# Kernel tuning notes

Hardware: AMD Instinct MI355X
Metric: run time of the kernel (lower is better)

The kernel has to match this reference:

```python
import jax, jax.numpy as jnp
import numpy as np

V = 49152      # HEALPix nside=64 pixel count
B = 2
FIN = 32
FOUT = 64
K = 8          # Chebyshev kernel_size
DEG = 8        # neighbors per pixel (plus self-loop -> 9 nnz/row)
G = 8          # GroupNorm num_groups
EPS = 1e-5
SLOPE = 0.1    # LeakyReLU negative slope


def setup_inputs() -> dict:
    key = jax.random.key(0)
    ks = jax.random.split(key, 4)
    rng = np.random.default_rng(0)
    # sparse Laplacian in COO: 8 random neighbors + self-loop per node
    row = np.repeat(np.arange(V, dtype=np.int32), DEG + 1)
    nbrs = rng.integers(0, V, size=(V, DEG))
    col = np.concatenate([nbrs, np.arange(V)[:, None]], axis=1).astype(np.int32).reshape(-1)
    vals = (rng.standard_normal(V * (DEG + 1)).astype(np.float32)) * 0.1
    x = jax.random.normal(ks[0], (B, V, FIN), dtype=jnp.float32)
    W1 = jax.random.normal(ks[1], (K, FIN, FOUT), dtype=jnp.float32) * 0.05
    W2 = jax.random.normal(ks[2], (K, FOUT, FOUT), dtype=jnp.float32) * 0.05
    Wr = jax.random.normal(ks[3], (K, FIN, FOUT), dtype=jnp.float32) * 0.05
    zeros = jnp.zeros((FOUT,), dtype=jnp.float32)
    ones = jnp.ones((FOUT,), dtype=jnp.float32)
    return {
        "x": x,
        "lap_vals": jnp.asarray(vals),
        "lap_row": jnp.asarray(row),
        "lap_col": jnp.asarray(col),
        "W1": W1, "b1": zeros, "g1": ones, "be1": zeros,
        "W2": W2, "b2": zeros, "g2": ones, "be2": zeros,
        "Wr": Wr, "br": zeros,
    }


def _spmm(vals, row, col, z):
    # L @ z for COO Laplacian; z: [V, D]
    return jax.ops.segment_sum(vals[:, None] * z[col], row, num_segments=V)


def _cheb_conv(x, vals, row, col, W, b):
    # x: [B, V, Fin], W: [K, Fin, Fout] -> [B, V, Fout]
    Bb, Vv, F = x.shape
    x0 = jnp.transpose(x, (1, 0, 2)).reshape(Vv, Bb * F)  # [V, B*F]
    xs = [x0, _spmm(vals, row, col, x0)]
    for _ in range(K - 2):
        xs.append(2.0 * _spmm(vals, row, col, xs[-1]) - xs[-2])
    Xk = jnp.stack(xs, 0).reshape(K, Vv, Bb, F)
    Xk = jnp.transpose(Xk, (2, 1, 0, 3))  # [B, V, K, F]
    return jnp.einsum('bvkf,kfo->bvo', Xk, W) + b


def _group_norm(x, gamma, beta):
    # equivalent to nn.GroupNorm applied on x.permute(0,2,1): normalize over (C/G, V)
    Bb, Vv, C = x.shape
    xg = x.reshape(Bb, Vv, G, C // G)
    mu = xg.mean(axis=(1, 3), keepdims=True)
    var = xg.var(axis=(1, 3), keepdims=True)
    xn = ((xg - mu) * jax.lax.rsqrt(var + EPS)).reshape(Bb, Vv, C)
    return xn * gamma + beta


def _block(x, vals, row, col, W, b, gamma, beta):
    h = _cheb_conv(x, vals, row, col, W, b)
    h = _group_norm(h, gamma, beta)
    return jax.nn.leaky_relu(h, SLOPE)  # out_channels > 1 -> LeakyReLU(0.1)


def reference(x, lap_vals, lap_row, lap_col, W1, b1, g1, be1, W2, b2, g2, be2, Wr, br):
    h = _block(x, lap_vals, lap_row, lap_col, W1, b1, g1, be1)
    h = _block(h, lap_vals, lap_row, lap_col, W2, b2, g2, be2)
    res = _cheb_conv(x, lap_vals, lap_row, lap_col, Wr, br)  # in != out -> res_conv
    return h + res
```

## Files before the change

### kernel.cpp

```cpp
#include <hip/hip_runtime.h>
#include <hip/hip_bf16.h>

#define V 49152
#define NNZ 9
#define EPSV 1e-5f
#define SLOPE 0.1f
#define RST 68

typedef __attribute__((ext_vector_type(8))) short bf16x8;
typedef __attribute__((ext_vector_type(4))) float f32x4;

__device__ __forceinline__ float lo2f(unsigned u) { return __uint_as_float(u << 16); }
__device__ __forceinline__ float hi2f(unsigned u) { return __uint_as_float(u & 0xffff0000u); }
__device__ __forceinline__ unsigned short f2us(float f) {
    __hip_bfloat16 h = __float2bfloat16(f);
    return *(unsigned short*)&h;
}
__device__ __forceinline__ unsigned pk2(float a, float b) {
    return ((unsigned)f2us(a)) | (((unsigned)f2us(b)) << 16);
}
__device__ __forceinline__ void fma8(float* t, float a, uint4 u) {
    t[0] += a * lo2f(u.x); t[1] += a * hi2f(u.x);
    t[2] += a * lo2f(u.y); t[3] += a * hi2f(u.y);
    t[4] += a * lo2f(u.z); t[5] += a * hi2f(u.z);
    t[6] += a * lo2f(u.w); t[7] += a * hi2f(u.w);
}
__device__ __forceinline__ void fold8(float* t, uint4 p) {
    t[0] = 2.f*t[0] - lo2f(p.x); t[1] = 2.f*t[1] - hi2f(p.x);
    t[2] = 2.f*t[2] - lo2f(p.y); t[3] = 2.f*t[3] - hi2f(p.y);
    t[4] = 2.f*t[4] - lo2f(p.z); t[5] = 2.f*t[5] - hi2f(p.z);
    t[6] = 2.f*t[6] - lo2f(p.w); t[7] = 2.f*t[7] - hi2f(p.w);
}
__device__ __forceinline__ uint4 pack8(const float* t) {
    uint4 r;
    r.x = pk2(t[0], t[1]); r.y = pk2(t[2], t[3]);
    r.z = pk2(t[4], t[5]); r.w = pk2(t[6], t[7]);
    return r;
}
__device__ __forceinline__ void gnleaky8(uint4 u, const float* scl, const float* sft, float* y) {
    float e[8] = { lo2f(u.x), hi2f(u.x), lo2f(u.y), hi2f(u.y),
                   lo2f(u.z), hi2f(u.z), lo2f(u.w), hi2f(u.w) };
    #pragma unroll
    for (int i = 0; i < 8; ++i) {
        float t = e[i] * scl[i] + sft[i];
        y[i] = t > 0.f ? t : SLOPE * t;
    }
}
__device__ __forceinline__ void gload_lds16(const void* g, void* l) {
    __builtin_amdgcn_global_load_lds((__attribute__((address_space(1))) void*)g,
                                     (__attribute__((address_space(3))) void*)l, 16, 0, 0);
}

__global__ __launch_bounds__(256) void prep_reorder_k(
    const float* __restrict__ x, unsigned* __restrict__ t0,
    const float* __restrict__ W1, const float* __restrict__ Wr, const float* __restrict__ W2,
    unsigned short* __restrict__ Wt1, unsigned short* __restrict__ Wtr, unsigned short* __restrict__ Wt2,
    float* __restrict__ part)
{
    int bid = blockIdx.x;
    if (bid < 6144) {
        int idx = bid * 256 + threadIdx.x;
        int v = idx >> 5, j2 = idx & 31;
        int b = j2 >> 4, f0 = (j2 & 15) * 2;
        const float* p = x + ((size_t)b * V + v) * 32 + f0;
        t0[idx] = pk2(p[0], p[1]);
    } else {
        int i = (bid - 6144) * 256 + threadIdx.x;
        if (i < 32768) {
            int kk = i >> 12, rem = i & 4095, o = rem >> 6, f = rem & 63;
            Wt2[i] = f2us(W2[kk * 4096 + f * 64 + o]);
        } else if (i < 49152) {
            int j = i - 32768;
            int kk = j >> 11, rem = j & 2047, o = rem >> 5, f = rem & 31;
            Wt1[j] = f2us(W1[kk * 2048 + f * 64 + o]);
        } else if (i < 65536) {
            int j = i - 49152;
            int kk = j >> 11, rem = j & 2047, o = rem >> 5, f = rem & 31;
            Wtr[j] = f2us(Wr[kk * 2048 + f * 64 + o]);
        } else if (i < 66560) {
            part[i - 65536] = 0.f;
        }
    }
}

template<int THR, bool FIRST>
__global__ __launch_bounds__(256) void spmm_step(
    const uint4* __restrict__ zc, const uint4* __restrict__ zp, uint4* __restrict__ zn,
    const float* __restrict__ vals, const int* __restrict__ col)
{
    constexpr int L4 = THR * 2;
    int tid = blockIdx.x * 256 + threadIdx.x;
    int v = tid / THR;
    int c = (tid - v * THR) * 2;
    int base = v * NNZ;
    float t[16];
    #pragma unroll
    for (int i = 0; i < 16; ++i) t[i] = 0.f;
    #pragma unroll
    for (int n = 0; n < NNZ; ++n) {
        float a = vals[base + n];
        int cc = col[base + n];
        const uint4* p = zc + (size_t)cc * L4 + c;
        fma8(t, a, p[0]);
        fma8(t + 8, a, p[1]);
    }
    if (!FIRST) {
        const uint4* pp = zp + (size_t)v * L4 + c;
        fold8(t, pp[0]);
        fold8(t + 8, pp[1]);
    }
    uint4* q = zn + (size_t)v * L4 + c;
    q[0] = pack8(t);
    q[1] = pack8(t + 8);
}

template<int MODE>
__global__ __launch_bounds__(256) void spmm2_gn(
    const unsigned short* __restrict__ ACC, const uint4* __restrict__ zc,
    uint4* __restrict__ zn, const float* __restrict__ part,
    const float* __restrict__ gamma, const float* __restrict__ beta,
    const float* __restrict__ vals, const int* __restrict__ col)
{
    int tid = blockIdx.x * 256 + threadIdx.x;
    int v = tid >> 3;
    int c2 = (tid & 7) * 2;
    int b = c2 >> 3;
    int ch0 = (c2 & 7) * 8;
    const float Nf = (float)V * 8.f;
    int g0 = c2 & 7;
    float m0 = part[(b*8+g0)*2] / Nf;
    float r0 = rsqrtf(part[(b*8+g0)*2+1]/Nf - m0*m0 + EPSV);
    float m1 = part[(b*8+g0+1)*2] / Nf;
    float r1 = rsqrtf(part[(b*8+g0+1)*2+1]/Nf - m1*m1 + EPSV);
    float scl[16], sft[16];
    #pragma unroll
    for (int i = 0; i < 8; ++i) {
        int o = ch0 + i;
        scl[i] = r0 * gamma[o];     sft[i] = beta[o] - m0 * scl[i];
        scl[8+i] = r1 * gamma[o+8]; sft[8+i] = beta[o+8] - m1 * scl[8+i];
    }

    float t[16];
    #pragma unroll
    for (int i = 0; i < 16; ++i) t[i] = 0.f;
    int base = v * NNZ;
    #pragma unroll
    for (int n = 0; n < NNZ; ++n) {
        float a = vals[base + n];
        int cc = col[base + n];
        if constexpr (MODE == 0) {
            const uint4* p = (const uint4*)(const void*)(ACC + ((size_t)b * V + cc) * 64 + ch0);
            float y[8];
            gnleaky8(p[0], scl, sft, y);
            #pragma unroll
            for (int i = 0; i < 8; ++i) t[i] += a * y[i];
            gnleaky8(p[1], scl + 8, sft + 8, y);
            #pragma unroll
            for (int i = 0; i < 8; ++i) t[8 + i] += a * y[i];
        } else {
            const uint4* p = zc + (size_t)cc * 16 + c2;
            fma8(t, a, p[0]);
            fma8(t + 8, a, p[1]);
        }
    }
    if constexpr (MODE == 1) {
        const uint4* pp = (const uint4*)(const void*)(ACC + ((size_t)b * V + v) * 64 + ch0);
        float y[8];
        gnleaky8(pp[0], scl, sft, y);
        #pragma unroll
        for (int i = 0; i < 8; ++i) t[i] = 2.f * t[i] - y[i];
        gnleaky8(pp[1], scl + 8, sft + 8, y);
        #pragma unroll
        for (int i = 0; i < 8; ++i) t[8 + i] = 2.f * t[8 + i] - y[i];
    }
    uint4* q = zn + (size_t)v * 16 + c2;
    q[0] = pack8(t);
    q[1] = pack8(t + 8);
}

__global__ __launch_bounds__(256) void gemm1f(
    const unsigned short* __restrict__ T,
    const unsigned short* __restrict__ WtA, const unsigned short* __restrict__ WtB,
    const float* __restrict__ biasA, const float* __restrict__ biasB,
    const float* __restrict__ vals, const int* __restrict__ col,
    unsigned short* __restrict__ ACC, float* __restrict__ resOut, float* __restrict__ part)
{
    __shared__ unsigned short shraw[34816];
    __shared__ float sGrp[32];
    unsigned short* tile = shraw;
    float* accbuf  = (float*)shraw;
    float* dualbuf = accbuf + 2 * 64 * RST;

    int wv = threadIdx.x >> 6, lane = threadIdx.x & 63;
    int quad = lane >> 4, l15 = lane & 15;
    int v0 = blockIdx.x * 64;
    int ot = wv;

    #pragma unroll
    for (int i = 0; i < 14; ++i) {
        int s = (i * 4 + wv) * 64 + lane;
        int kkl = s >> 9;
        int ws = s & 511;
        int row = ws >> 3;
        int cl = ws & 7;
        int cg = cl ^ (row & 7);
        const unsigned short* gp = T + ((size_t)kkl * V + v0 + row) * 64 + cg * 8;
        gload_lds16(gp, tile + (size_t)(i * 4 + wv) * 64 * 8);
    }

    {
        const unsigned short* T6 = T + (size_t)6 * V * 64;
        const unsigned short* T5 = T + (size_t)5 * V * 64;
        int row = threadIdx.x >> 2, c2 = (threadIdx.x & 3) * 2;
        int gv = v0 + row;
        float t[16];
        #pragma unroll
        for (int i = 0; i < 16; ++i) t[i] = 0.f;
        int base = gv * NNZ;
        #pragma unroll
        for (int n = 0; n < NNZ; ++n) {
            float a = vals[base + n];
            int cc = col[base + n];
            const uint4* p = (const uint4*)(const void*)(T6 + (size_t)cc * 64 + c2 * 8);
            fma8(t, a, p[0]);
            fma8(t + 8, a, p[1]);
        }
        const uint4* pp = (const uint4*)(const void*)(T5 + (size_t)gv * 64 + c2 * 8);
        fold8(t, pp[0]);
        fold8(t + 8, pp[1]);
        uint4* tl = (uint4*)tile;
        int r7 = row & 7;
        tl[(7 * 64 + row) * 8 + (c2 ^ r7)]       = pack8(t);
        tl[(7 * 64 + row) * 8 + ((c2 + 1) ^ r7)] = pack8(t + 8);
    }

    bf16x8 bw[8], bd[8];
    #pragma unroll
    for (int kk = 0; kk < 8; ++kk) {
        size_t brow = ((size_t)kk * 64 + ot * 16 + l15) * 32 + quad * 8;
        bw[kk] = *(const bf16x8*)(const void*)(WtA + brow);
        bd[kk] = *(const bf16x8*)(const void*)(WtB + brow);
    }
    f32x4 acc[4][2], accd[4][2];
    #pragma unroll
    for (int m = 0; m < 4; ++m)
        #pragma unroll
        for (int b = 0; b < 2; ++b) {
            acc[m][b]  = (f32x4){0.f, 0.f, 0.f, 0.f};
            accd[m][b] = (f32x4){0.f, 0.f, 0.f, 0.f};
        }
    __syncthreads();

    #pragma unroll
    for (int kk = 0; kk < 8; ++kk) {
        #pragma unroll
        for (int m = 0; m < 4; ++m) {
            int r = m * 16 + l15;
            int rx = r & 7;
            const unsigned short* rbase = tile + ((size_t)kk * 64 + r) * 64;
            #pragma unroll
            for (int b = 0; b < 2; ++b) {
                int s0 = (b * 4 + quad) ^ rx;
                bf16x8 a = *(const bf16x8*)(const void*)(rbase + s0 * 8);
                acc[m][b]  = __builtin_amdgcn_mfma_f32_16x16x32_bf16(a, bw[kk], acc[m][b], 0, 0, 0);
                accd[m][b] = __builtin_amdgcn_mfma_f32_16x16x32_bf16(a, bd[kk], accd[m][b], 0, 0, 0);
            }
        }
    }

    __syncthreads();
    int o = ot * 16 + l15;
    float biA = biasA[o], biB = biasB[o];
    #pragma unroll
    for (int m = 0; m < 4; ++m)
        #pragma unroll
        for (int b = 0; b < 2; ++b)
            #pragma unroll
            for (int rr = 0; rr < 4; ++rr) {
                int r = m * 16 + quad * 4 + rr;
                accbuf[(b * 64 + r) * RST + o] = acc[m][b][rr] + biA;
                dualbuf[(b * 64 + r) * RST + o] = accd[m][b][rr] + biB;
            }
    if (threadIdx.x < 32) sGrp[threadIdx.x] = 0.f;
    __syncthreads();
    #pragma unroll
    for (int j = 0; j < 4; ++j) {
        int cid = threadIdx.x + 256 * j;
        int g = cid & 7, r = (cid >> 3) & 63, b = cid >> 9;
        const float* src = accbuf + (b * 64 + r) * RST + g * 8;
        float e[8], s = 0.f, q = 0.f;
        #pragma unroll
        for (int i = 0; i < 8; ++i) { e[i] = src[i]; s += e[i]; q += e[i] * e[i]; }
        *(uint4*)(void*)(ACC + ((size_t)b * V + v0 + r) * 64 + g * 8) = pack8(e);
        atomicAdd(&sGrp[b * 8 + g], s);
        atomicAdd(&sGrp[16 + b * 8 + g], q);
    }
    #pragma unroll
    for (int j = 0; j < 8; ++j) {
        int cid = threadIdx.x + 256 * j;
        int oc = cid & 15, r = (cid >> 4) & 63, b = cid >> 10;
        float4 vv = *(const float4*)(const void*)(dualbuf + (b * 64 + r) * RST + oc * 4);
        *(float4*)(void*)(resOut + ((size_t)b * V + v0 + r) * 64 + oc * 4) = vv;
    }
    __syncthreads();
    if (threadIdx.x < 16) {
        atomicAdd(&part[threadIdx.x * 2],     sGrp[threadIdx.x]);
        atomicAdd(&part[threadIdx.x * 2 + 1], sGrp[16 + threadIdx.x]);
    }
}

__global__ __launch_bounds__(256) void gemm2f(
    const unsigned short* __restrict__ T,
    unsigned short* ACC,
    const float* __restrict__ part1, const float* __restrict__ g1, const float* __restrict__ be1,
    const unsigned short* __restrict__ Wt2, const float* __restrict__ biasA,
    float* __restrict__ part2,
    const float* __restrict__ vals, const int* __restrict__ col)
{
    __shared__ unsigned short shraw[32768];
    __shared__ float sGrp[32];
    unsigned short* tile = shraw;
    float* accbuf = (float*)shraw;

    int wv = threadIdx.x >> 6, lane = threadIdx.x & 63;
    int quad = lane >> 4, l15 = lane & 15;
    int v0 = blockIdx.x * 64;
    int ot = wv;
    const float Nf = (float)V * 8.f;

    #pragma unroll
    for (int i = 4; i < 16; ++i) {
        int s = (i * 4 + wv) * 64 + lane;
        int kkl = s >> 10;
        int ws = s & 1023;
        int row = ws >> 4;
        int cl = ws & 15;
        int cg = (cl & ~7) | ((cl & 7) ^ (row & 7));
        const unsigned short* gp = T + ((size_t)kkl * V + v0 + row) * 128 + cg * 8;
        gload_lds16(gp, tile + (size_t)(i * 4 + wv) * 64 * 8);
    }
    {
        int cl = threadIdx.x & 15;
        int b = cl >> 3, g = cl & 7, j8 = b * 8 + g;
        float mean = part1[j8 * 2] / Nf;
        float rstd = rsqrtf(part1[j8 * 2 + 1] / Nf - mean * mean + EPSV);
        int o0 = g * 8;
        float scl[8], sft[8];
        #pragma unroll
        for (int i = 0; i < 8; ++i) {
            scl[i] = rstd * g1[o0 + i];
            sft[i] = be1[o0 + i] - mean * scl[i];
        }
        uint4* tl = (uint4*)tile;
        #pragma unroll
        for (int j = 0; j < 4; ++j) {
            int r = (threadIdx.x >> 4) + 16 * j;
            uint4 aa = *(const uint4*)(const void*)(ACC + ((size_t)b * V + v0 + r) * 64 + o0);
            float y[8];
            gnleaky8(aa, scl, sft, y);
            tl[r * 16 + ((cl & ~7) | ((cl & 7) ^ (r & 7)))] = pack8(y);
        }
    }
    bf16x8 bw[8][2];
    #pragma unroll
    for (int kk = 0; kk < 8; ++kk)
        #pragma unroll
        for (int fh = 0; fh < 2; ++fh) {
            size_t brow = ((size_t)kk * 64 + ot * 16 + l15) * 64 + fh * 32 + quad * 8;
            bw[kk][fh] = *(const bf16x8*)(const void*)(Wt2 + brow);
        }
    f32x4 acc[4][2];
    #pragma unroll
    for (int m = 0; m < 4; ++m)
        #pragma unroll
        for (int b = 0; b < 2; ++b) acc[m][b] = (f32x4){0.f, 0.f, 0.f, 0.f};
    __syncthreads();

    #pragma unroll
    for (int kkl = 0; kkl < 4; ++kkl) {
        #pragma unroll
        for (int m = 0; m < 4; ++m) {
            int r = m * 16 + l15, rx = r & 7;
            const unsigned short* rbase = tile + ((size_t)kkl * 64 + r) * 128;
            #pragma unroll
            for (int b = 0; b < 2; ++b)
                #pragma unroll
                for (int fh = 0; fh < 2; ++fh) {
                    int c0 = b * 8 + fh * 4 + quad;
                    int s0 = (c0 & ~7) | ((c0 & 7) ^ rx);
                    bf16x8 a = *(const bf16x8*)(const void*)(rbase + s0 * 8);
                    acc[m][b] = __builtin_amdgcn_mfma_f32_16x16x32_bf16(a, bw[kkl][fh], acc[m][b], 0, 0, 0);
                }
        }
    }
    __syncthreads();

    #pragma unroll
    for (int i = 0; i < 12; ++i) {
        int s = (i * 4 + wv) * 64 + lane;
        int kkl = s >> 10;
        int ws = s & 1023;
        int row = ws >> 4;
        int cl = ws & 15;
        int cg = (cl & ~7) | ((cl & 7) ^ (row & 7));
        const unsigned short* gp = T + ((size_t)(4 + kkl) * V + v0 + row) * 128 + cg * 8;
        gload_lds16(gp, tile + (size_t)(i * 4 + wv) * 64 * 8);
    }
    {
        const unsigned short* T6 = T + (size_t)6 * V * 128;
        const unsigned short* T5 = T + (size_t)5 * V * 128;
        int row = threadIdx.x >> 2, cb = (threadIdx.x & 3) * 4;
        int gv = v0 + row;
        float t[32];
        #pragma unroll
        for (int i = 0; i < 32; ++i) t[i] = 0.f;
        int base = gv * NNZ;
        #pragma unroll
        for (int n = 0; n < NNZ; ++n) {
            float a = vals[base + n];
            int cc = col[base + n];
            const uint4* p = (const uint4*)(const void*)(T6 + (size_t)cc * 128 + cb * 8);
            fma8(t, a, p[0]);
            fma8(t + 8, a, p[1]);
            fma8(t + 16, a, p[2]);
            fma8(t + 24, a, p[3]);
        }
        const uint4* pp = (const uint4*)(const void*)(T5 + (size_t)gv * 128 + cb * 8);
        fold8(t, pp[0]);
        fold8(t + 8, pp[1]);
        fold8(t + 16, pp[2]);
        fold8(t + 24, pp[3]);
        uint4* tl = (uint4*)tile;
        int r7 = row & 7;
        #pragma unroll
        for (int q = 0; q < 4; ++q) {
            int c = cb + q;
            tl[(3 * 64 + row) * 16 + ((c & ~7) | ((c & 7) ^ r7))] = pack8(t + q * 8);
        }
    }
    __syncthreads();

    #pragma unroll
    for (int kkl = 0; kkl < 4; ++kkl) {
        int kk = 4 + kkl;
        #pragma unroll
        for (int m = 0; m < 4; ++m) {
            int r = m * 16 + l15, rx = r & 7;
            const unsigned short* rbase = tile + ((size_t)kkl * 64 + r) * 128;
            #pragma unroll
            for (int b = 0; b < 2; ++b)
                #pragma unroll
                for (int fh = 0; fh < 2; ++fh) {
                    int c0 = b * 8 + fh * 4 + quad;
                    int s0 = (c0 & ~7) | ((c0 & 7) ^ rx);
                    bf16x8 a = *(const bf16x8*)(const void*)(rbase + s0 * 8);
                    acc[m][b] = __builtin_amdgcn_mfma_f32_16x16x32_bf16(a, bw[kk][fh], acc[m][b], 0, 0, 0);
                }
        }
    }

    __syncthreads();
    int o = ot * 16 + l15;
    float biA = biasA[o];
    #pragma unroll
    for (int m = 0; m < 4; ++m)
        #pragma unroll
        for (int b = 0; b < 2; ++b)
            #pragma unroll
            for (int rr = 0; rr < 4; ++rr) {
                int r = m * 16 + quad * 4 + rr;
                accbuf[(b * 64 + r) * RST + o] = acc[m][b][rr] + biA;
            }
    if (threadIdx.x < 32) sGrp[threadIdx.x] = 0.f;
    __syncthreads();
    #pragma unroll
    for (int j = 0; j < 4; ++j) {
        int cid = threadIdx.x + 256 * j;
        int g = cid & 7, r = (cid >> 3) & 63, b = cid >> 9;
        const float* src = accbuf + (b * 64 + r) * RST + g * 8;
        float e[8], s = 0.f, q = 0.f;
        #pragma unroll
        for (int i = 0; i < 8; ++i) { e[i] = src[i]; s += e[i]; q += e[i] * e[i]; }
        *(uint4*)(void*)(ACC + ((size_t)b * V + v0 + r) * 64 + g * 8) = pack8(e);
        atomicAdd(&sGrp[b * 8 + g], s);
        atomicAdd(&sGrp[16 + b * 8 + g], q);
    }
    __syncthreads();
    if (threadIdx.x < 16) {
        atomicAdd(&part2[threadIdx.x * 2],     sGrp[threadIdx.x]);
        atomicAdd(&part2[threadIdx.x * 2 + 1], sGrp[16 + threadIdx.x]);
    }
}

__global__ __launch_bounds__(256) void final_out(const unsigned short* __restrict__ ACC,
                                                 float* outres,
                                                 const float* __restrict__ part,
                                                 const float* __restrict__ gamma, const float* __restrict__ beta) {
    int idx = blockIdx.x * 256 + threadIdx.x;
    int b = idx >= V * 8 ? 1 : 0;
    int r = idx - b * V * 8;
    int v = r >> 3, g = r & 7;
    int j = b * 8 + g;
    const float N = (float)V * 8.f;
    float mean = part[j * 2] / N;
    float rstd = rsqrtf(part[j * 2 + 1] / N - mean * mean + EPSV);
    int o0 = g * 8;
    size_t base = ((size_t)b * V + v) * 64 + o0;
    uint4 aa = *(const uint4*)(const void*)(ACC + base);
    float e[8] = { lo2f(aa.x), hi2f(aa.x), lo2f(aa.y), hi2f(aa.y),
                   lo2f(aa.z), hi2f(aa.z), lo2f(aa.w), hi2f(aa.w) };
    float4 r0 = *(const float4*)(const void*)(outres + base);
    float4 r1 = *(const float4*)(const void*)(outres + base + 4);
    float y[8];
    #pragma unroll
    for (int i = 0; i < 8; ++i) {
        float t = (e[i] - mean) * rstd * gamma[o0 + i] + beta[o0 + i];
        y[i] = t > 0.f ? t : SLOPE * t;
    }
    float4 w0 = { y[0] + r0.x, y[1] + r0.y, y[2] + r0.z, y[3] + r0.w };
    float4 w1 = { y[4] + r1.x, y[5] + r1.y, y[6] + r1.z, y[7] + r1.w };
    *(float4*)(void*)(outres + base) = w0;
    *(float4*)(void*)(outres + base + 4) = w1;
}

extern "C" void kernel_launch(void* const* d_in, const int* in_sizes, int n_in,
                              void* d_out, int out_size, void* d_ws, size_t ws_size,
                              hipStream_t stream) {
    const float* x    = (const float*)d_in[0];
    const float* vals = (const float*)d_in[1];
    const int*   col  = (const int*)d_in[3];
    const float* W1   = (const float*)d_in[4];
    const float* b1   = (const float*)d_in[5];
    const float* g1   = (const float*)d_in[6];
    const float* be1  = (const float*)d_in[7];
    const float* W2   = (const float*)d_in[8];
    const float* b2   = (const float*)d_in[9];
    const float* g2   = (const float*)d_in[10];
    const float* be2  = (const float*)d_in[11];
    const float* Wr   = (const float*)d_in[12];
    const float* br   = (const float*)d_in[13];
    float* out = (float*)d_out;

    unsigned short* TS  = (unsigned short*)d_ws;
    unsigned short* ACC = TS + (size_t)8 * V * 128;
    unsigned short* Wt1 = ACC + (size_t)2 * V * 64;
    unsigned short* Wtr = Wt1 + 8 * 64 * 32;
    unsigned short* Wt2 = Wtr + 8 * 64 * 32;
    float* PART1 = (float*)(Wt2 + 8 * 64 * 64);
    float* PART2 = PART1 + 32;

    prep_reorder_k<<<6404, 256, 0, stream>>>(x, (unsigned*)TS, W1, Wr, W2, Wt1, Wtr, Wt2, PART1);

    uint4* T1s[8];
    for (int k = 0; k < 8; ++k) T1s[k] = (uint4*)(TS + (size_t)k * V * 64);
    spmm_step<4, true><<<V * 4 / 256, 256, 0, stream>>>(T1s[0], nullptr, T1s[1], vals, col);
    for (int k = 2; k < 7; ++k)
        spmm_step<4, false><<<V * 4 / 256, 256, 0, stream>>>(T1s[k-1], T1s[k-2], T1s[k], vals, col);

    gemm1f<<<V / 64, 256, 0, stream>>>(TS, Wt1, Wtr, b1, br, vals, col, ACC, out, PART1);

    uint4* T2s[8];
    for (int k = 0; k < 8; ++k) T2s[k] = (uint4*)(TS + (size_t)k * V * 128);
    spmm2_gn<0><<<V * 8 / 256, 256, 0, stream>>>(ACC, nullptr, T2s[1], PART1, g1, be1, vals, col);
    spmm2_gn<1><<<V * 8 / 256, 256, 0, stream>>>(ACC, T2s[1], T2s[2], PART1, g1, be1, vals, col);
    for (int k = 3; k < 7; ++k)
        spmm_step<8, false><<<V * 8 / 256, 256, 0, stream>>>(T2s[k-1], T2s[k-2], T2s[k], vals, col);

    gemm2f<<<V / 64, 256, 0, stream>>>(TS, ACC, PART1, g1, be1, Wt2, b2, PART2, vals, col);

    final_out<<<2 * V * 8 / 256, 256, 0, stream>>>(ACC, out, PART2, g2, be2);
}
```

Baseline: 364.1 us.

## Double-buffer LDS staging in GEMM kernels and store residual as bf16

Both fused GEMM kernels now stage one or two Chebyshev terms at a time into two ping-pong LDS buffers instead of loading the whole tile up front. Compute on one buffer overlaps loads into the other. The much smaller shared-memory footprint, together with launch-bound occupancy hints, is meant to fit more blocks per CU. The epilogue is split into per-batch passes so it fits the smaller LDS. The residual conv output is written as a bf16 intermediate instead of fp32 into the output, which cuts traffic but adds a rounding step to the residual path.

```diff
diff --git a/kernel.cpp b/kernel.cpp
--- a/kernel.cpp
+++ b/kernel.cpp
@@ -50,6 +50,33 @@
     __builtin_amdgcn_global_load_lds((__attribute__((address_space(1))) void*)g,
                                      (__attribute__((address_space(3))) void*)l, 16, 0, 0);
 }
+
+#define EPI_PASS(SRCM, PB, BI, DSTPTR, DOSTATS)                                     \
+    {                                                                               \
+        __syncthreads();                                                            \
+        _Pragma("unroll")                                                           \
+        for (int m_ = 0; m_ < 4; ++m_)                                              \
+            _Pragma("unroll")                                                       \
+            for (int rr_ = 0; rr_ < 4; ++rr_) {                                     \
+                int r_ = m_ * 16 + quad * 4 + rr_;                                  \
+                epi[r_ * RST + o] = SRCM[m_][PB][rr_] + (BI);                       \
+            }                                                                       \
+        __syncthreads();                                                            \
+        _Pragma("unroll")                                                           \
+        for (int j_ = 0; j_ < 2; ++j_) {                                            \
+            int cid_ = (int)threadIdx.x + 256 * j_;                                 \
+            int g_ = cid_ & 7, r_ = cid_ >> 3;                                      \
+            const float* src_ = epi + r_ * RST + g_ * 8;                            \
+            float e_[8], s_ = 0.f, q_ = 0.f;                                        \
+            _Pragma("unroll")                                                       \
+            for (int i_ = 0; i_ < 8; ++i_) { e_[i_] = src_[i_]; s_ += e_[i_]; q_ += e_[i_] * e_[i_]; } \
+            *(uint4*)(void*)((DSTPTR) + ((size_t)(PB) * V + v0 + r_) * 64 + g_ * 8) = pack8(e_); \
+            if (DOSTATS) {                                                          \
+                atomicAdd(&sGrp[(PB) * 8 + g_], s_);                                \
+                atomicAdd(&sGrp[16 + (PB) * 8 + g_], q_);                           \
+            }                                                                       \
+        }                                                                           \
+    }
 
 __global__ __launch_bounds__(256) void prep_reorder_k(
     const float* __restrict__ x, unsigned* __restrict__ t0,
@@ -77,7 +104,7 @@
             int j = i - 49152;
             int kk = j >> 11, rem = j & 2047, o = rem >> 5, f = rem & 31;
             Wtr[j] = f2us(Wr[kk * 2048 + f * 64 + o]);
-        } else if (i < 66560) {
+        } else if (i < 65600) {
             part[i - 65536] = 0.f;
         }
     }
@@ -178,86 +205,42 @@
     q[1] = pack8(t + 8);
 }
 
-__global__ __launch_bounds__(256) void gemm1f(
+__global__ __launch_bounds__(256, 3) void gemm1f(
     const unsigned short* __restrict__ T,
     const unsigned short* __restrict__ WtA, const unsigned short* __restrict__ WtB,
     const float* __restrict__ biasA, const float* __restrict__ biasB,
     const float* __restrict__ vals, const int* __restrict__ col,
-    unsigned short* __restrict__ ACC, float* __restrict__ resOut, float* __restrict__ part)
+    unsigned short* __restrict__ ACC, unsigned short* __restrict__ RES, float* __restrict__ part)
 {
-    __shared__ unsigned short shraw[34816];
+    __shared__ __align__(16) unsigned short shraw[16384];
     __shared__ float sGrp[32];
-    unsigned short* tile = shraw;
-    float* accbuf  = (float*)shraw;
-    float* dualbuf = accbuf + 2 * 64 * RST;
+    float* epi = (float*)shraw;
+    unsigned short* bA = shraw;
+    unsigned short* bB = shraw + 8192;
 
     int wv = threadIdx.x >> 6, lane = threadIdx.x & 63;
     int quad = lane >> 4, l15 = lane & 15;
     int v0 = blockIdx.x * 64;
     int ot = wv;
 
-    #pragma unroll
-    for (int i = 0; i < 14; ++i) {
-        int s = (i * 4 + wv) * 64 + lane;
-        int kkl = s >> 9;
-        int ws = s & 511;
-        int row = ws >> 3;
-        int cl = ws & 7;
-        int cg = cl ^ (row & 7);
-        const unsigned short* gp = T + ((size_t)kkl * V + v0 + row) * 64 + cg * 8;
-        gload_lds16(gp, tile + (size_t)(i * 4 + wv) * 64 * 8);
-    }
-
-    {
-        const unsigned short* T6 = T + (size_t)6 * V * 64;
-        const unsigned short* T5 = T + (size_t)5 * V * 64;
-        int row = threadIdx.x >> 2, c2 = (threadIdx.x & 3) * 2;
-        int gv = v0 + row;
-        float t[16];
-        #pragma unroll
-        for (int i = 0; i < 16; ++i) t[i] = 0.f;
-        int base = gv * NNZ;
-        #pragma unroll
-        for (int n = 0; n < NNZ; ++n) {
-            float a = vals[base + n];
-            int cc = col[base + n];
-            const uint4* p = (const uint4*)(const void*)(T6 + (size_t)cc * 64 + c2 * 8);
-            fma8(t, a, p[0]);
-            fma8(t + 8, a, p[1]);
-        }
-        const uint4* pp = (const uint4*)(const void*)(T5 + (size_t)gv * 64 + c2 * 8);
-        fold8(t, pp[0]);
-        fold8(t + 8, pp[1]);
-        uint4* tl = (uint4*)tile;
-        int r7 = row & 7;
-        tl[(7 * 64 + row) * 8 + (c2 ^ r7)]       = pack8(t);
-        tl[(7 * 64 + row) * 8 + ((c2 + 1) ^ r7)] = pack8(t + 8);
-    }
+    auto stage = [&](int kk, unsigned short* dst) {
+        #pragma unroll
+        for (int i = 0; i < 2; ++i) {
+            int s = (i * 4 + wv) * 64 + lane;
+            int row = s >> 3, cl = s & 7;
+            int cg = cl ^ (row & 7);
+            const unsigned short* gp = T + ((size_t)kk * V + v0 + row) * 64 + cg * 8;
+            gload_lds16(gp, dst + (size_t)(i * 4 + wv) * 64 * 8);
+        }
+    };
 
     bf16x8 bw[8], bd[8];
-    #pragma unroll
-    for (int kk = 0; kk < 8; ++kk) {
-        size_t brow = ((size_t)kk * 64 + ot * 16 + l15) * 32 + quad * 8;
-        bw[kk] = *(const bf16x8*)(const void*)(WtA + brow);
-        bd[kk] = *(const bf16x8*)(const void*)(WtB + brow);
-    }
     f32x4 acc[4][2], accd[4][2];
-    #pragma unroll
-    for (int m = 0; m < 4; ++m)
-        #pragma unroll
-        for (int b = 0; b < 2; ++b) {
-            acc[m][b]  = (f32x4){0.f, 0.f, 0.f, 0.f};
-            accd[m][b] = (f32x4){0.f, 0.f, 0.f, 0.f};
-        }
-    __syncthreads();
-
-    #pragma unroll
-    for (int kk = 0; kk < 8; ++kk) {
+    auto comp = [&](int kk, const unsigned short* sb) {
         #pragma unroll
         for (int m = 0; m < 4; ++m) {
-            int r = m * 16 + l15;
-            int rx = r & 7;
-            const unsigned short* rbase = tile + ((size_t)kk * 64 + r) * 64;
+            int r = m * 16 + l15, rx = r & 7;
+            const unsigned short* rbase = sb + (size_t)r * 64;
             #pragma unroll
             for (int b = 0; b < 2; ++b) {
                 int s0 = (b * 4 + quad) ^ rx;
@@ -266,42 +249,70 @@
                 accd[m][b] = __builtin_amdgcn_mfma_f32_16x16x32_bf16(a, bd[kk], accd[m][b], 0, 0, 0);
             }
         }
-    }
-
-    __syncthreads();
+    };
+
+    stage(0, bA); stage(1, bA + 4096);
+    #pragma unroll
+    for (int kk = 0; kk < 8; ++kk) {
+        size_t brow = ((size_t)kk * 64 + ot * 16 + l15) * 32 + quad * 8;
+        bw[kk] = *(const bf16x8*)(const void*)(WtA + brow);
+        bd[kk] = *(const bf16x8*)(const void*)(WtB + brow);
+    }
+    #pragma unroll
+    for (int m = 0; m < 4; ++m)
+        #pragma unroll
+        for (int b = 0; b < 2; ++b) {
+            acc[m][b]  = (f32x4){0.f, 0.f, 0.f, 0.f};
+            accd[m][b] = (f32x4){0.f, 0.f, 0.f, 0.f};
+        }
+    __syncthreads();
+
+    stage(2, bB); stage(3, bB + 4096);
+    comp(0, bA); comp(1, bA + 4096);
+    __syncthreads();
+
+    stage(4, bA); stage(5, bA + 4096);
+    comp(2, bB); comp(3, bB + 4096);
+    __syncthreads();
+
+    stage(6, bB);
+    {
+        const unsigned short* T6 = T + (size_t)6 * V * 64;
+        const unsigned short* T5 = T + (size_t)5 * V * 64;
+        int row = threadIdx.x >> 2, c2 = (threadIdx.x & 3) * 2;
+        int gv = v0 + row;
+        float t[16];
+        #pragma unroll
+        for (int i = 0; i < 16; ++i) t[i] = 0.f;
+        int base = gv * NNZ;
+        #pragma unroll
+        for (int n = 0; n < NNZ; ++n) {
+            float a = vals[base + n];
+            int cc = col[base + n];
+            const uint4* p = (const uint4*)(const void*)(T6 + (size_t)cc * 64 + c2 * 8);
+            fma8(t, a, p[0]);
+            fma8(t + 8, a, p[1]);
+        }
+        const uint4* pp = (const uint4*)(const void*)(T5 + (size_t)gv * 64 + c2 * 8);
+        fold8(t, pp[0]);
+        fold8(t + 8, pp[1]);
+        uint4* tl = (uint4*)(bB + 4096);
+        int r7 = row & 7;
+        comp(4, bA); comp(5, bA + 4096);
+        tl[row * 8 + (c2 ^ r7)]       = pack8(t);
+        tl[row * 8 + ((c2 + 1) ^ r7)] = pack8(t + 8);
+    }
+    __syncthreads();
+
+    comp(6, bB); comp(7, bB + 4096);
+
+    if (threadIdx.x < 32) sGrp[threadIdx.x] = 0.f;
     int o = ot * 16 + l15;
     float biA = biasA[o], biB = biasB[o];
-    #pragma unroll
-    for (int m = 0; m < 4; ++m)
-        #pragma unroll
-        for (int b = 0; b < 2; ++b)
-            #pragma unroll
-            for (int rr = 0; rr < 4; ++rr) {
-                int r = m * 16 + quad * 4 + rr;
-                accbuf[(b * 64 + r) * RST + o] = acc[m][b][rr] + biA;
-                dualbuf[(b * 64 + r) * RST + o] = accd[m][b][rr] + biB;
-            }
-    if (threadIdx.x < 32) sGrp[threadIdx.x] = 0.f;
-    __syncthreads();
-    #pragma unroll
-    for (int j = 0; j < 4; ++j) {
-        int cid = threadIdx.x + 256 * j;
-        int g = cid & 7, r = (cid >> 3) & 63, b = cid >> 9;
-        const float* src = accbuf + (b * 64 + r) * RST + g * 8;
-        float e[8], s = 0.f, q = 0.f;
-        #pragma unroll
-        for (int i = 0; i < 8; ++i) { e[i] = src[i]; s += e[i]; q += e[i] * e[i]; }
-        *(uint4*)(void*)(ACC + ((size_t)b * V + v0 + r) * 64 + g * 8) = pack8(e);
-        atomicAdd(&sGrp[b * 8 + g], s);
-        atomicAdd(&sGrp[16 + b * 8 + g], q);
-    }
-    #pragma unroll
-    for (int j = 0; j < 8; ++j) {
-        int cid = threadIdx.x + 256 * j;
-        int oc = cid & 15, r = (cid >> 4) & 63, b = cid >> 10;
-        float4 vv = *(const float4*)(const void*)(dualbuf + (b * 64 + r) * RST + oc * 4);
-        *(float4*)(void*)(resOut + ((size_t)b * V + v0 + r) * 64 + oc * 4) = vv;
-    }
+    EPI_PASS(acc,  0, biA, ACC, true)
+    EPI_PASS(acc,  1, biA, ACC, true)
+    EPI_PASS(accd, 0, biB, RES, false)
+    EPI_PASS(accd, 1, biB, RES, false)
     __syncthreads();
     if (threadIdx.x < 16) {
         atomicAdd(&part[threadIdx.x * 2],     sGrp[threadIdx.x]);
@@ -309,7 +320,7 @@
     }
 }
 
-__global__ __launch_bounds__(256) void gemm2f(
+__global__ __launch_bounds__(256, 4) void gemm2f(
     const unsigned short* __restrict__ T,
     unsigned short* ACC,
     const float* __restrict__ part1, const float* __restrict__ g1, const float* __restrict__ be1,
@@ -317,10 +328,11 @@
     float* __restrict__ part2,
     const float* __restrict__ vals, const int* __restrict__ col)
 {
-    __shared__ unsigned short shraw[32768];
+    __shared__ __align__(16) unsigned short shraw[16384];
     __shared__ float sGrp[32];
-    unsigned short* tile = shraw;
-    float* accbuf = (float*)shraw;
+    float* epi = (float*)shraw;
+    unsigned short* b0 = shraw;
+    unsigned short* b1 = shraw + 8192;
 
     int wv = threadIdx.x >> 6, lane = threadIdx.x & 63;
     int quad = lane >> 4, l15 = lane & 15;
@@ -328,125 +340,24 @@
     int ot = wv;
     const float Nf = (float)V * 8.f;
 
-    #pragma unroll
-    for (int i = 4; i < 16; ++i) {
-        int s = (i * 4 + wv) * 64 + lane;
-        int kkl = s >> 10;
-        int ws = s & 1023;
-        int row = ws >> 4;
-        int cl = ws & 15;
-        int cg = (cl & ~7) | ((cl & 7) ^ (row & 7));
-        const unsigned short* gp = T + ((size_t)kkl * V + v0 + row) * 128 + cg * 8;
-        gload_lds16(gp, tile + (size_t)(i * 4 + wv) * 64 * 8);
-    }
-    {
-        int cl = threadIdx.x & 15;
-        int b = cl >> 3, g = cl & 7, j8 = b * 8 + g;
-        float mean = part1[j8 * 2] / Nf;
-        float rstd = rsqrtf(part1[j8 * 2 + 1] / Nf - mean * mean + EPSV);
-        int o0 = g * 8;
-        float scl[8], sft[8];
-        #pragma unroll
-        for (int i = 0; i < 8; ++i) {
-            scl[i] = rstd * g1[o0 + i];
-            sft[i] = be1[o0 + i] - mean * scl[i];
-        }
-        uint4* tl = (uint4*)tile;
-        #pragma unroll
-        for (int j = 0; j < 4; ++j) {
-            int r = (threadIdx.x >> 4) + 16 * j;
-            uint4 aa = *(const uint4*)(const void*)(ACC + ((size_t)b * V + v0 + r) * 64 + o0);
-            float y[8];
-            gnleaky8(aa, scl, sft, y);
-            tl[r * 16 + ((cl & ~7) | ((cl & 7) ^ (r & 7)))] = pack8(y);
-        }
-    }
+    auto stage = [&](int kk, unsigned short* dst) {
+        #pragma unroll
+        for (int i = 0; i < 4; ++i) {
+            int s = (i * 4 + wv) * 64 + lane;
+            int row = s >> 4, cl = s & 15;
+            int cg = (cl & ~7) | ((cl & 7) ^ (row & 7));
+            const unsigned short* gp = T + ((size_t)kk * V + v0 + row) * 128 + cg * 8;
+            gload_lds16(gp, dst + (size_t)(i * 4 + wv) * 64 * 8);
+        }
+    };
+
     bf16x8 bw[8][2];
-    #pragma unroll
-    for (int kk = 0; kk < 8; ++kk)
-        #pragma unroll
-        for (int fh = 0; fh < 2; ++fh) {
-            size_t brow = ((size_t)kk * 64 + ot * 16 + l15) * 64 + fh * 32 + quad * 8;
-            bw[kk][fh] = *(const bf16x8*)(const void*)(Wt2 + brow);
-        }
     f32x4 acc[4][2];
-    #pragma unroll
-    for (int m = 0; m < 4; ++m)
-        #pragma unroll
-        for (int b = 0; b < 2; ++b) acc[m][b] = (f32x4){0.f, 0.f, 0.f, 0.f};
-    __syncthreads();
-
-    #pragma unroll
-    for (int kkl = 0; kkl < 4; ++kkl) {
+    auto comp = [&](int kk, const unsigned short* sb) {
         #pragma unroll
         for (int m = 0; m < 4; ++m) {
             int r = m * 16 + l15, rx = r & 7;
-            const unsigned short* rbase = tile + ((size_t)kkl * 64 + r) * 128;
-            #pragma unroll
-            for (int b = 0; b < 2; ++b)
-                #pragma unroll
-                for (int fh = 0; fh < 2; ++fh) {
-                    int c0 = b * 8 + fh * 4 + quad;
-                    int s0 = (c0 & ~7) | ((c0 & 7) ^ rx);
-                    bf16x8 a = *(const bf16x8*)(const void*)(rbase + s0 * 8);
-                    acc[m][b] = __builtin_amdgcn_mfma_f32_16x16x32_bf16(a, bw[kkl][fh], acc[m][b], 0, 0, 0);
-                }
-        }
-    }
-    __syncthreads();
-
-    #pragma unroll
-    for (int i = 0; i < 12; ++i) {
-        int s = (i * 4 + wv) * 64 + lane;
-        int kkl = s >> 10;
-        int ws = s & 1023;
-        int row = ws >> 4;
-        int cl = ws & 15;
-        int cg = (cl & ~7) | ((cl & 7) ^ (row & 7));
-        const unsigned short* gp = T + ((size_t)(4 + kkl) * V + v0 + row) * 128 + cg * 8;
-        gload_lds16(gp, tile + (size_t)(i * 4 + wv) * 64 * 8);
-    }
-    {
-        const unsigned short* T6 = T + (size_t)6 * V * 128;
-        const unsigned short* T5 = T + (size_t)5 * V * 128;
-        int row = threadIdx.x >> 2, cb = (threadIdx.x & 3) * 4;
-        int gv = v0 + row;
-        float t[32];
-        #pragma unroll
-        for (int i = 0; i < 32; ++i) t[i] = 0.f;
-        int base = gv * NNZ;
-        #pragma unroll
-        for (int n = 0; n < NNZ; ++n) {
-            float a = vals[base + n];
-            int cc = col[base + n];
-            const uint4* p = (const uint4*)(const void*)(T6 + (size_t)cc * 128 + cb * 8);
-            fma8(t, a, p[0]);
-            fma8(t + 8, a, p[1]);
-            fma8(t + 16, a, p[2]);
-            fma8(t + 24, a, p[3]);
-        }
-        const uint4* pp = (const uint4*)(const void*)(T5 + (size_t)gv * 128 + cb * 8);
-        fold8(t, pp[0]);
-        fold8(t + 8, pp[1]);
-        fold8(t + 16, pp[2]);
-        fold8(t + 24, pp[3]);
-        uint4* tl = (uint4*)tile;
-        int r7 = row & 7;
-        #pragma unroll
-        for (int q = 0; q < 4; ++q) {
-            int c = cb + q;
-            tl[(3 * 64 + row) * 16 + ((c & ~7) | ((c & 7) ^ r7))] = pack8(t + q * 8);
-        }
-    }
-    __syncthreads();
-
-    #pragma unroll
-    for (int kkl = 0; kkl < 4; ++kkl) {
-        int kk = 4 + kkl;
-        #pragma unroll
-        for (int m = 0; m < 4; ++m) {
-            int r = m * 16 + l15, rx = r & 7;
-            const unsigned short* rbase = tile + ((size_t)kkl * 64 + r) * 128;
+            const unsigned short* rbase = sb + (size_t)r * 128;
             #pragma unroll
             for (int b = 0; b < 2; ++b)
                 #pragma unroll
@@ -457,34 +368,97 @@
                     acc[m][b] = __builtin_amdgcn_mfma_f32_16x16x32_bf16(a, bw[kk][fh], acc[m][b], 0, 0, 0);
                 }
         }
-    }
-
-    __syncthreads();
+    };
+
+    stage(1, b1);
+    {
+        int cl = threadIdx.x & 15;
+        int b = cl >> 3, g = cl & 7, j8 = b * 8 + g;
+        float mean = part1[j8 * 2] / Nf;
+        float rstd = rsqrtf(part1[j8 * 2 + 1] / Nf - mean * mean + EPSV);
+        int o0 = g * 8;
+        float scl[8], sft[8];
+        #pragma unroll
+        for (int i = 0; i < 8; ++i) {
+            scl[i] = rstd * g1[o0 + i];
+            sft[i] = be1[o0 + i] - mean * scl[i];
+        }
+        uint4* tl = (uint4*)b0;
+        #pragma unroll
+        for (int j = 0; j < 4; ++j) {
+            int r = (threadIdx.x >> 4) + 16 * j;
+            uint4 aa = *(const uint4*)(const void*)(ACC + ((size_t)b * V + v0 + r) * 64 + o0);
+            float y[8];
+            gnleaky8(aa, scl, sft, y);
+            tl[r * 16 + ((cl & ~7) | ((cl & 7) ^ (r & 7)))] = pack8(y);
+        }
+    }
+    #pragma unroll
+    for (int kk = 0; kk < 8; ++kk)
+        #pragma unroll
+        for (int fh = 0; fh < 2; ++fh) {
+            size_t brow = ((size_t)kk * 64 + ot * 16 + l15) * 64 + fh * 32 + quad * 8;
+            bw[kk][fh] = *(const bf16x8*)(const void*)(Wt2 + brow);
+        }
+    #pragma unroll
+    for (int m = 0; m < 4; ++m)
+        #pragma unroll
+        for (int b = 0; b < 2; ++b) acc[m][b] = (f32x4){0.f, 0.f, 0.f, 0.f};
+    __syncthreads();
+
+    comp(0, b0);
+    __syncthreads();
+    stage(2, b0); comp(1, b1);
+    __syncthreads();
+    stage(3, b1); comp(2, b0);
+    __syncthreads();
+    stage(4, b0); comp(3, b1);
+    __syncthreads();
+    stage(5, b1); comp(4, b0);
+    __syncthreads();
+    stage(6, b0); comp(5, b1);
+    __syncthreads();
+    {
+        const unsigned short* T6 = T + (size_t)6 * V * 128;
+        const unsigned short* T5 = T + (size_t)5 * V * 128;
+        int row = threadIdx.x >> 2, cb = (threadIdx.x & 3) * 4;
+        int gv = v0 + row;
+        float t[32];
+        #pragma unroll
+        for (int i = 0; i < 32; ++i) t[i] = 0.f;
+        int base = gv * NNZ;
+        #pragma unroll
+        for (int n = 0; n < NNZ; ++n) {
+            float a = vals[base + n];
+            int cc = col[base + n];
+            const uint4* p = (const uint4*)(const void*)(T6 + (size_t)cc * 128 + cb * 8);
+            fma8(t, a, p[0]);
+            fma8(t + 8, a, p[1]);
+            fma8(t + 16, a, p[2]);
+            fma8(t + 24, a, p[3]);
+        }
+        const uint4* pp = (const uint4*)(const void*)(T5 + (size_t)gv * 128 + cb * 8);
+        fold8(t, pp[0]);
+        fold8(t + 8, pp[1]);
+        fold8(t + 16, pp[2]);
+        fold8(t + 24, pp[3]);
+        uint4* tl = (uint4*)b1;
+        int r7 = row & 7;
+        #pragma unroll
+        for (int q = 0; q < 4; ++q) {
+            int c = cb + q;
+            tl[row * 16 + ((c & ~7) | ((c & 7) ^ r7))] = pack8(t + q * 8);
+        }
+        comp(6, b0);
+    }
+    __syncthreads();
+    comp(7, b1);
+
+    if (threadIdx.x < 32) sGrp[threadIdx.x] = 0.f;
     int o = ot * 16 + l15;
     float biA = biasA[o];
-    #pragma unroll
-    for (int m = 0; m < 4; ++m)
-        #pragma unroll
-        for (int b = 0; b < 2; ++b)
-            #pragma unroll
-            for (int rr = 0; rr < 4; ++rr) {
-                int r = m * 16 + quad * 4 + rr;
-                accbuf[(b * 64 + r) * RST + o] = acc[m][b][rr] + biA;
-            }
-    if (threadIdx.x < 32) sGrp[threadIdx.x] = 0.f;
-    __syncthreads();
-    #pragma unroll
-    for (int j = 0; j < 4; ++j) {
-        int cid = threadIdx.x + 256 * j;
-        int g = cid & 7, r = (cid >> 3) & 63, b = cid >> 9;
-        const float* src = accbuf + (b * 64 + r) * RST + g * 8;
-        float e[8], s = 0.f, q = 0.f;
-        #pragma unroll
-        for (int i = 0; i < 8; ++i) { e[i] = src[i]; s += e[i]; q += e[i] * e[i]; }
-        *(uint4*)(void*)(ACC + ((size_t)b * V + v0 + r) * 64 + g * 8) = pack8(e);
-        atomicAdd(&sGrp[b * 8 + g], s);
-        atomicAdd(&sGrp[16 + b * 8 + g], q);
-    }
+    EPI_PASS(acc, 0, biA, ACC, true)
+    EPI_PASS(acc, 1, biA, ACC, true)
     __syncthreads();
     if (threadIdx.x < 16) {
         atomicAdd(&part2[threadIdx.x * 2],     sGrp[threadIdx.x]);
@@ -493,7 +467,8 @@
 }
 
 __global__ __launch_bounds__(256) void final_out(const unsigned short* __restrict__ ACC,
-                                                 float* outres,
+                                                 const unsigned short* __restrict__ RES,
+                                                 float* __restrict__ out,
                                                  const float* __restrict__ part,
                                                  const float* __restrict__ gamma, const float* __restrict__ beta) {
     int idx = blockIdx.x * 256 + threadIdx.x;
@@ -507,20 +482,21 @@
     int o0 = g * 8;
     size_t base = ((size_t)b * V + v) * 64 + o0;
     uint4 aa = *(const uint4*)(const void*)(ACC + base);
+    uint4 rr = *(const uint4*)(const void*)(RES + base);
     float e[8] = { lo2f(aa.x), hi2f(aa.x), lo2f(aa.y), hi2f(aa.y),
                    lo2f(aa.z), hi2f(aa.z), lo2f(aa.w), hi2f(aa.w) };
-    float4 r0 = *(const float4*)(const void*)(outres + base);
-    float4 r1 = *(const float4*)(const void*)(outres + base + 4);
+    float re[8] = { lo2f(rr.x), hi2f(rr.x), lo2f(rr.y), hi2f(rr.y),
+                    lo2f(rr.z), hi2f(rr.z), lo2f(rr.w), hi2f(rr.w) };
     float y[8];
     #pragma unroll
     for (int i = 0; i < 8; ++i) {
         float t = (e[i] - mean) * rstd * gamma[o0 + i] + beta[o0 + i];
-        y[i] = t > 0.f ? t : SLOPE * t;
-    }
-    float4 w0 = { y[0] + r0.x, y[1] + r0.y, y[2] + r0.z, y[3] + r0.w };
-    float4 w1 = { y[4] + r1.x, y[5] + r1.y, y[6] + r1.z, y[7] + r1.w };
-    *(float4*)(void*)(outres + base) = w0;
-    *(float4*)(void*)(outres + base + 4) = w1;
+        y[i] = (t > 0.f ? t : SLOPE * t) + re[i];
+    }
+    float4 w0 = { y[0], y[1], y[2], y[3] };
+    float4 w1 = { y[4], y[5], y[6], y[7] };
+    *(float4*)(void*)(out + base) = w0;
+    *(float4*)(void*)(out + base + 4) = w1;
 }
 
 extern "C" void kernel_launch(void* const* d_in, const int* in_sizes, int n_in,
@@ -543,7 +519,8 @@
 
     unsigned short* TS  = (unsigned short*)d_ws;
     unsigned short* ACC = TS + (size_t)8 * V * 128;
-    unsigned short* Wt1 = ACC + (size_t)2 * V * 64;
+    unsigned short* RES = ACC + (size_t)2 * V * 64;
+    unsigned short* Wt1 = RES + (size_t)2 * V * 64;
     unsigned short* Wtr = Wt1 + 8 * 64 * 32;
     unsigned short* Wt2 = Wtr + 8 * 64 * 32;
     float* PART1 = (float*)(Wt2 + 8 * 64 * 64);
@@ -557,7 +534,7 @@
     for (int k = 2; k < 7; ++k)
         spmm_step<4, false><<<V * 4 / 256, 256, 0, stream>>>(T1s[k-1], T1s[k-2], T1s[k], vals, col);
 
-    gemm1f<<<V / 64, 256, 0, stream>>>(TS, Wt1, Wtr, b1, br, vals, col, ACC, out, PART1);
+    gemm1f<<<V / 64, 256, 0, stream>>>(TS, Wt1, Wtr, b1, br, vals, col, ACC, RES, PART1);
 
     uint4* T2s[8];
     for (int k = 0; k < 8; ++k) T2s[k] = (uint4*)(TS + (size_t)k * V * 128);
@@ -568,5 +545,5 @@
 
     gemm2f<<<V / 64, 256, 0, stream>>>(TS, ACC, PART1, g1, be1, Wt2, b2, PART2, vals, col);
 
-    final_out<<<2 * V * 8 / 256, 256, 0, stream>>>(ACC, out, PART2, g2, be2);
-}
+    final_out<<<2 * V * 8 / 256, 256, 0, stream>>>(ACC, RES, out, PART2, g2, be2);
+}
```

New measurement: 395.5 us. 8.6% more time.
